# Kernel optimization log

Measured on AMD Instinct MI355X. Metric: run time of the kernel, lower is better.

## Reference

```python
import jax, jax.numpy as jnp
import numpy as np

B, LD, HD, CC, SC, PN, MAX_N = 256, 256, 512, 64, 256, 100000, 128


def setup_inputs() -> dict:
    key = jax.random.key(0)
    ks = jax.random.split(key, 24)
    def W(k, i, o):
        return jax.random.normal(k, (i, o), jnp.float32) * 0.02
    latent = jax.random.normal(ks[0], (B, LD), jnp.float32)
    n = jax.random.randint(ks[1], (B,), 0, MAX_N, jnp.int32)
    points = jax.random.normal(ks[2], (PN, SC), jnp.float32)
    a = jax.random.normal(ks[3], (PN, CC), jnp.float32)
    angles_params = a / (jnp.linalg.norm(a, axis=1, keepdims=True) + 1e-5)
    return {
        "latent": latent, "n": n, "points": points, "angles_params": angles_params,
        # angle_mlp: LD->HD->HD->HD->CC (4 linears, relu between)
        "aw1": W(ks[4], LD, HD), "ab1": jnp.zeros((HD,), jnp.float32),
        "aw2": W(ks[5], HD, HD), "ab2": jnp.zeros((HD,), jnp.float32),
        "aw3": W(ks[6], HD, HD), "ab3": jnp.zeros((HD,), jnp.float32),
        "aw4": W(ks[7], HD, CC), "ab4": jnp.zeros((CC,), jnp.float32),
        # lin1/lin2: 1 -> SC
        "l1w": W(ks[8], 1, SC), "l1b": jnp.zeros((SC,), jnp.float32),
        "l2w": W(ks[9], 1, SC), "l2b": jnp.zeros((SC,), jnp.float32),
        # out_lin: (SC+LD)->(SC+LD)->SC->SC
        "ow1": W(ks[10], SC + LD, SC + LD), "ob1": jnp.zeros((SC + LD,), jnp.float32),
        "ow2": W(ks[11], SC + LD, SC), "ob2": jnp.zeros((SC,), jnp.float32),
        "ow3": W(ks[12], SC, SC), "ob3": jnp.zeros((SC,), jnp.float32),
    }


def reference(latent, n, points, angles_params,
              aw1, ab1, aw2, ab2, aw3, ab3, aw4, ab4,
              l1w, l1b, l2w, l2b,
              ow1, ob1, ow2, ob2, ow3, ob3):
    n_r = jnp.clip(n, 1, MAX_N)  # round_n
    # angle_mlp
    h = jax.nn.relu(latent @ aw1 + ab1)
    h = jax.nn.relu(h @ aw2 + ab2)
    h = jax.nn.relu(h @ aw3 + ab3)
    ang = h @ aw4 + ab4                                   # [B, CC]
    ang = ang / (jnp.linalg.norm(ang, axis=1, keepdims=True) + 1e-5)
    cosine = jax.nn.softmax(ang @ angles_params.T, axis=1)  # [B, PN]
    srted, idx = jax.lax.top_k(cosine, MAX_N)             # sorted descending
    sel = points[idx]                                     # [B, MAX_N, SC] gather
    s = (MAX_N * srted)[..., None]                        # [B, MAX_N, 1]
    alpha = s @ l1w + l1b
    beta = s @ l2w + l2b
    mod = alpha * sel + beta                              # [B, MAX_N, SC]
    mask = (jnp.arange(MAX_N)[None, :] < n_r[:, None]).astype(jnp.float32)[..., None]
    cat = jnp.concatenate(
        [mod, jnp.broadcast_to(latent[:, None, :], (latent.shape[0], MAX_N, latent.shape[1]))],
        axis=-1)
    o = jax.nn.relu(cat @ ow1 + ob1)
    o = jax.nn.relu(o @ ow2 + ob2)
    out = o @ ow3 + ob3                                   # [B, MAX_N, SC]
    return out, mask, n_r
```

## Files before the change

kernel.cpp:

```cpp
#include <hip/hip_runtime.h>

#define PN 100000
#define NCB2 1563
#define NCBG 782
#define TSEL 0.33f
#define NSLOT 8
#define PREP_AP 3128
#define PREP_TOT 4408
#define PREP_CHUNK 1102

typedef _Float16 f16;
typedef _Float16 f16x8 __attribute__((ext_vector_type(8)));
typedef _Float16 f16x4 __attribute__((ext_vector_type(4)));
typedef float f32x4 __attribute__((ext_vector_type(4)));

__device__ __forceinline__ unsigned int sortkey(float f) {
    unsigned int u = __float_as_uint(f);
    return u ^ ((u & 0x80000000u) ? 0xFFFFFFFFu : 0x80000000u);
}

__device__ __forceinline__ void gload_lds16(const void* g, void* l) {
    __builtin_amdgcn_global_load_lds((const __attribute__((address_space(1))) void*)g,
                                     (__attribute__((address_space(3))) void*)l, 16, 0, 0);
}

__device__ __forceinline__ void prep_work(
    int pid, const float* __restrict__ ap, f16* __restrict__ apHpre, f16* __restrict__ apLpre,
    const float* __restrict__ ow1, const float* __restrict__ ow2, const float* __restrict__ ow3,
    f16* __restrict__ W1t, f16* __restrict__ W2t, f16* __restrict__ W3t)
{
    if (pid < PREP_AP) {
        int idx = pid * 256 + threadIdx.x;
        int gcol = idx >> 3, m = idx & 7;
        int bx = gcol >> 7, col = gcol & 127;
        size_t woff = (size_t)bx * 16384 + (size_t)col * 128 + (size_t)((m ^ (col & 7)) << 4);
        f16x8 h, l;
        if (gcol < PN) {
            const float* src = &ap[(size_t)gcol * 64 + m * 8];
            float4 a = *(const float4*)&src[0];
            float4 b = *(const float4*)&src[4];
            h[0] = (f16)a.x; l[0] = (f16)(a.x - (float)h[0]);
            h[1] = (f16)a.y; l[1] = (f16)(a.y - (float)h[1]);
            h[2] = (f16)a.z; l[2] = (f16)(a.z - (float)h[2]);
            h[3] = (f16)a.w; l[3] = (f16)(a.w - (float)h[3]);
            h[4] = (f16)b.x; l[4] = (f16)(b.x - (float)h[4]);
            h[5] = (f16)b.y; l[5] = (f16)(b.y - (float)h[5]);
            h[6] = (f16)b.z; l[6] = (f16)(b.z - (float)h[6]);
            h[7] = (f16)b.w; l[7] = (f16)(b.w - (float)h[7]);
        } else {
            h = (f16x8){}; l = (f16x8){};
        }
        *(f16x8*)((char*)apHpre + woff) = h;
        *(f16x8*)((char*)apLpre + woff) = l;
    } else {
        int idx = (pid - PREP_AP) * 256 + threadIdx.x;
        if (idx < 131072) {
            int n = idx >> 8, k = idx & 255;
            W1t[idx] = (f16)ow1[(size_t)k * 512 + n];
        } else if (idx < 262144) {
            int j = idx - 131072;
            int n = j >> 9, k = j & 511;
            W2t[j] = (f16)ow2[(size_t)k * 256 + n];
        } else {
            int j = idx - 262144;
            int n = j >> 8, k = j & 255;
            W3t[j] = (f16)ow3[(size_t)k * 256 + n];
        }
    }
}

template<int RELU>
__global__ __launch_bounds__(256) void k1_layer(
    const float* __restrict__ X, const float* __restrict__ W,
    const float* __restrict__ bias, float* __restrict__ Y,
    int N, int K, int prep_base,
    const float* __restrict__ ap, f16* __restrict__ apHpre, f16* __restrict__ apLpre,
    const float* __restrict__ ow1, const float* __restrict__ ow2, const float* __restrict__ ow3,
    f16* __restrict__ W1t, f16* __restrict__ W2t, f16* __restrict__ W3t)
{
    int bid = blockIdx.x;
    if (bid >= 128) {
        prep_work(prep_base + bid - 128, ap, apHpre, apLpre, ow1, ow2, ow3, W1t, W2t, W3t);
        return;
    }
    __shared__ __align__(16) float As[128][36];
    __shared__ __align__(16) float Bs[128][36];
    int t = threadIdx.x;
    int cbase = (bid & 15) * 32;
    int rbase = (bid >> 4) * 32;
    int tx = t & 7, ty = t >> 3;
    float acc[4] = {};

    for (int kt = 0; kt < K; kt += 128) {
        #pragma unroll
        for (int i = 0; i < 4; ++i) {
            int e = i * 256 + t;
            int r = e >> 5, k4 = e & 31;
            float4 v = *(const float4*)&X[(size_t)(rbase + r) * K + kt + k4 * 4];
            As[k4 * 4 + 0][r] = v.x; As[k4 * 4 + 1][r] = v.y;
            As[k4 * 4 + 2][r] = v.z; As[k4 * 4 + 3][r] = v.w;
        }
        #pragma unroll
        for (int i = 0; i < 4; ++i) {
            int e = i * 256 + t;
            int k = e >> 3, c4 = e & 7;
            *(float4*)&Bs[k][c4 * 4] = *(const float4*)&W[(size_t)(kt + k) * N + cbase + c4 * 4];
        }
        __syncthreads();
        #pragma unroll 8
        for (int k = 0; k < 128; ++k) {
            float av = As[k][ty];
            float4 bv = *(const float4*)&Bs[k][tx * 4];
            acc[0] = fmaf(av, bv.x, acc[0]);
            acc[1] = fmaf(av, bv.y, acc[1]);
            acc[2] = fmaf(av, bv.z, acc[2]);
            acc[3] = fmaf(av, bv.w, acc[3]);
        }
        __syncthreads();
    }
    int row = rbase + ty;
    #pragma unroll
    for (int j = 0; j < 4; ++j) {
        int col = cbase + tx * 4 + j;
        float v = acc[j] + bias[col];
        Y[(size_t)row * N + col] = RELU ? fmaxf(v, 0.f) : v;
    }
}

__global__ __launch_bounds__(256) void k1_tail(
    const float* __restrict__ X, const float* __restrict__ W4,
    const float* __restrict__ b4, f16* __restrict__ angH, f16* __restrict__ angL,
    const float* __restrict__ latent, const float* __restrict__ ow1lat,
    const float* __restrict__ ob1, float* __restrict__ Lc, int prep_base,
    const float* __restrict__ ap, f16* __restrict__ apHpre, f16* __restrict__ apLpre,
    const float* __restrict__ ow1, const float* __restrict__ ow2, const float* __restrict__ ow3,
    f16* __restrict__ W1t, f16* __restrict__ W2t, f16* __restrict__ W3t)
{
    if (blockIdx.x >= 72) {
        prep_work(prep_base + blockIdx.x - 72, ap, apHpre, apLpre, ow1, ow2, ow3, W1t, W2t, W3t);
        return;
    }
    __shared__ __align__(16) float As[128][36];
    __shared__ __align__(16) float Bs[128][68];
    int t = threadIdx.x;
    int tx = t & 15, ty = t >> 4;
    float acc[2][4] = {};

    if (blockIdx.x < 8) {
        int rbase = blockIdx.x * 32;
        for (int kt = 0; kt < 512; kt += 128) {
            #pragma unroll
            for (int i = 0; i < 4; ++i) {
                int e = i * 256 + t;
                int r = e >> 5, k4 = e & 31;
                float4 v = *(const float4*)&X[(size_t)(rbase + r) * 512 + kt + k4 * 4];
                As[k4 * 4 + 0][r] = v.x; As[k4 * 4 + 1][r] = v.y;
                As[k4 * 4 + 2][r] = v.z; As[k4 * 4 + 3][r] = v.w;
            }
            #pragma unroll
            for (int i = 0; i < 8; ++i) {
                int e = i * 256 + t;
                int k = e >> 4, c4 = e & 15;
                *(float4*)&Bs[k][c4 * 4] = *(const float4*)&W4[(size_t)(kt + k) * 64 + c4 * 4];
            }
            __syncthreads();
            #pragma unroll 8
            for (int k = 0; k < 128; ++k) {
                float2 av = *(const float2*)&As[k][ty * 2];
                float4 bv = *(const float4*)&Bs[k][tx * 4];
                acc[0][0] = fmaf(av.x, bv.x, acc[0][0]); acc[0][1] = fmaf(av.x, bv.y, acc[0][1]);
                acc[0][2] = fmaf(av.x, bv.z, acc[0][2]); acc[0][3] = fmaf(av.x, bv.w, acc[0][3]);
                acc[1][0] = fmaf(av.y, bv.x, acc[1][0]); acc[1][1] = fmaf(av.y, bv.y, acc[1][1]);
                acc[1][2] = fmaf(av.y, bv.z, acc[1][2]); acc[1][3] = fmaf(av.y, bv.w, acc[1][3]);
            }
            __syncthreads();
        }
        #pragma unroll
        for (int i = 0; i < 2; ++i) {
            float v[4];
            float ss = 0.f;
            #pragma unroll
            for (int j = 0; j < 4; ++j) {
                v[j] = acc[i][j] + b4[tx * 4 + j];
                ss = fmaf(v[j], v[j], ss);
            }
            ss += __shfl_xor(ss, 1); ss += __shfl_xor(ss, 2);
            ss += __shfl_xor(ss, 4); ss += __shfl_xor(ss, 8);
            float inv = 1.0f / (sqrtf(ss) + 1e-5f);
            int row = rbase + ty * 2 + i;
            f16x4 h, l;
            #pragma unroll
            for (int j = 0; j < 4; ++j) {
                float val = v[j] * inv;
                h[j] = (f16)val;
                l[j] = (f16)(val - (float)h[j]);
            }
            *(f16x4*)&angH[(size_t)row * 64 + tx * 4] = h;
            *(f16x4*)&angL[(size_t)row * 64 + tx * 4] = l;
        }
    } else {
        int bid = blockIdx.x - 8;
        int cbase = (bid & 7) * 64;
        int rbase = (bid >> 3) * 32;
        for (int kt = 0; kt < 256; kt += 128) {
            #pragma unroll
            for (int i = 0; i < 4; ++i) {
                int e = i * 256 + t;
                int r = e >> 5, k4 = e & 31;
                float4 v = *(const float4*)&latent[(size_t)(rbase + r) * 256 + kt + k4 * 4];
                As[k4 * 4 + 0][r] = v.x; As[k4 * 4 + 1][r] = v.y;
                As[k4 * 4 + 2][r] = v.z; As[k4 * 4 + 3][r] = v.w;
            }
            #pragma unroll
            for (int i = 0; i < 8; ++i) {
                int e = i * 256 + t;
                int k = e >> 4, c4 = e & 15;
                *(float4*)&Bs[k][c4 * 4] = *(const float4*)&ow1lat[(size_t)(kt + k) * 512 + cbase + c4 * 4];
            }
            __syncthreads();
            #pragma unroll 8
            for (int k = 0; k < 128; ++k) {
                float2 av = *(const float2*)&As[k][ty * 2];
                float4 bv = *(const float4*)&Bs[k][tx * 4];
                acc[0][0] = fmaf(av.x, bv.x, acc[0][0]); acc[0][1] = fmaf(av.x, bv.y, acc[0][1]);
                acc[0][2] = fmaf(av.x, bv.z, acc[0][2]); acc[0][3] = fmaf(av.x, bv.w, acc[0][3]);
                acc[1][0] = fmaf(av.y, bv.x, acc[1][0]); acc[1][1] = fmaf(av.y, bv.y, acc[1][1]);
                acc[1][2] = fmaf(av.y, bv.z, acc[1][2]); acc[1][3] = fmaf(av.y, bv.w, acc[1][3]);
            }
            __syncthreads();
        }
        #pragma unroll
        for (int i = 0; i < 2; ++i) {
            int row = rbase + ty * 2 + i;
            #pragma unroll
            for (int j = 0; j < 4; ++j) {
                int col = cbase + tx * 4 + j;
                Lc[(size_t)row * 512 + col] = acc[i][j] + ob1[col];
            }
        }
    }
}

__global__ __launch_bounds__(256) void k2v10(
    const f16* __restrict__ angH, const f16* __restrict__ angL,
    const f16* __restrict__ apHpre, const f16* __restrict__ apLpre,
    float* __restrict__ gsum, unsigned int* __restrict__ cnt_g,
    unsigned long long* __restrict__ slot_g)
{
    __shared__ __align__(16) f16 Bh[128 * 64], Bl[128 * 64];
    __shared__ float psum[64][2];
    int t = threadIdx.x;
    int lane = t & 63, wave = t >> 6;
    int bx = blockIdx.x;
    int cbase = bx * 128;
    int rbase = blockIdx.y * 64;
    int wr = wave >> 1, wc = wave & 1;

    {
        const char* srcH = (const char*)apHpre + (size_t)bx * 16384 + t * 16;
        const char* srcL = (const char*)apLpre + (size_t)bx * 16384 + t * 16;
        char* dstH = (char*)Bh + wave * 1024;
        char* dstL = (char*)Bl + wave * 1024;
        #pragma unroll
        for (int c = 0; c < 4; ++c) {
            gload_lds16(srcH + c * 4096, dstH + c * 4096);
            gload_lds16(srcL + c * 4096, dstL + c * 4096);
        }
    }
    __syncthreads();

    f32x4 acc[2][4] = {};
    #pragma unroll
    for (int ks = 0; ks < 2; ++ks) {
        int kk = ks * 32 + (lane >> 4) * 8;
        f16x8 ah[2], al[2], bh[4], bl[4];
        #pragma unroll
        for (int i = 0; i < 2; ++i) {
            int row = rbase + wr * 32 + i * 16 + (lane & 15);
            ah[i] = *(const f16x8*)&angH[(size_t)row * 64 + kk];
            al[i] = *(const f16x8*)&angL[(size_t)row * 64 + kk];
        }
        #pragma unroll
        for (int j = 0; j < 4; ++j) {
            int col = wc * 64 + j * 16 + (lane & 15);
            unsigned int offb = (unsigned int)(col * 128 + kk * 2) ^ (unsigned int)((col & 7) << 4);
            bh[j] = *(const f16x8*)((char*)Bh + offb);
            bl[j] = *(const f16x8*)((char*)Bl + offb);
        }
        #pragma unroll
        for (int i = 0; i < 2; ++i)
            #pragma unroll
            for (int j = 0; j < 4; ++j) {
                acc[i][j] = __builtin_amdgcn_mfma_f32_16x16x32_f16(ah[i], bh[j], acc[i][j], 0, 0, 0);
                acc[i][j] = __builtin_amdgcn_mfma_f32_16x16x32_f16(ah[i], bl[j], acc[i][j], 0, 0, 0);
                acc[i][j] = __builtin_amdgcn_mfma_f32_16x16x32_f16(al[i], bh[j], acc[i][j], 0, 0, 0);
            }
    }

    int tx = lane & 15;
    #pragma unroll
    for (int i = 0; i < 2; ++i) {
        #pragma unroll
        for (int r2 = 0; r2 < 4; ++r2) {
            int lrow = wr * 32 + i * 16 + ((lane >> 4) << 2) + r2;
            int grow = rbase + lrow;
            float s = 0.f;
            unsigned int lk[4], li[4];
            int c = 0;
            #pragma unroll
            for (int j = 0; j < 4; ++j) {
                int gc = cbase + wc * 64 + j * 16 + tx;
                if (gc < PN) {
                    float v = acc[i][j][r2];
                    s += __expf(v);
                    if (v >= TSEL) { lk[c] = sortkey(v); li[c] = (unsigned int)gc; ++c; }
                }
            }
            s += __shfl_xor(s, 1); s += __shfl_xor(s, 2);
            s += __shfl_xor(s, 4); s += __shfl_xor(s, 8);
            int incl = c;
            #pragma unroll
            for (int d = 1; d < 16; d <<= 1) {
                int up = __shfl_up(incl, (unsigned int)d, 16);
                if (tx >= d) incl += up;
            }
            int excl = incl - c;
            int unit = bx * 2 + wc;
            if (unit < NCB2) {
                size_t base = ((size_t)unit * 256 + grow) * NSLOT;
                for (int k = 0; k < c; ++k) {
                    int sp = excl + k;
                    if (sp < NSLOT)
                        slot_g[base + sp] = (((unsigned long long)lk[k]) << 32) | (unsigned int)(~li[k]);
                }
                if (tx == 15) cnt_g[(size_t)unit * 256 + grow] = (unsigned int)incl;
            }
            if (tx == 0) psum[lrow][wc] = s;
        }
    }
    __syncthreads();
    if (t < 64)
        gsum[(size_t)bx * 256 + rbase + t] = psum[t][0] + psum[t][1];
}

__global__ __launch_bounds__(1024) void k3v5(
    const unsigned int* __restrict__ cnt_g, const unsigned long long* __restrict__ slot_g,
    const float* __restrict__ gsum, const int* __restrict__ nin,
    const float* __restrict__ points,
    const float* __restrict__ l1w, const float* __restrict__ l1b,
    const float* __restrict__ l2w, const float* __restrict__ l2b,
    f16* __restrict__ Xmod, float* __restrict__ maskp, float* __restrict__ nrp)
{
    __shared__ float wsum[16];
    __shared__ float s_inv;
    __shared__ unsigned int ccnt;
    __shared__ unsigned long long arr[1024];
    __shared__ float sprob[128];
    __shared__ int spi[128];
    __shared__ float sw1[256], sb1[256], sw2[256], sb2[256];

    int r = blockIdx.x;
    int t = threadIdx.x;
    if (t == 0) ccnt = 0u;
    if (t < 256) { sw1[t] = l1w[t]; sb1[t] = l1b[t]; sw2[t] = l2w[t]; sb2[t] = l2b[t]; }
    float es = 0.f;
    for (int i = t; i < NCBG; i += 1024) es += gsum[(size_t)i * 256 + r];
    #pragma unroll
    for (int off = 32; off > 0; off >>= 1) es += __shfl_xor(es, off);
    if ((t & 63) == 0) wsum[t >> 6] = es;
    __syncthreads();
    if (t == 0) {
        float s = 0.f;
        for (int i = 0; i < 16; ++i) s += wsum[i];
        s_inv = 1.0f / s;
    }
    for (int i = t; i < NCB2; i += 1024) {
        unsigned int c = cnt_g[(size_t)i * 256 + r];
        if (c) {
            c = min(c, (unsigned int)NSLOT);
            unsigned int p = atomicAdd(&ccnt, c);
            size_t base = ((size_t)i * 256 + r) * NSLOT;
            for (unsigned int k = 0; k < c; ++k)
                if (p + k < 1024u) arr[p + k] = slot_g[base + k];
        }
    }
    __syncthreads();
    int nc = (int)min(ccnt, 1024u);
    int P = 128;
    while (P < nc) P <<= 1;
    for (int i = t; i < P; i += 1024)
        if (i >= nc) arr[i] = 0ull;
    __syncthreads();
    for (int kk = 2; kk <= P; kk <<= 1) {
        for (int j = kk >> 1; j > 0; j >>= 1) {
            if (t < P) {
                int l = t ^ j;
                if (l > t) {
                    unsigned long long a = arr[t], b = arr[l];
                    bool up = ((t & kk) == 0);
                    if (up ? (a < b) : (a > b)) { arr[t] = b; arr[l] = a; }
                }
            }
            __syncthreads();
        }
    }
    int nr = nin[r]; nr = nr < 1 ? 1 : (nr > 128 ? 128 : nr);
    if (t < 128) {
        unsigned long long c = arr[t];
        unsigned int key = (unsigned int)(c >> 32);
        unsigned int idx = ~((unsigned int)c);
        if (idx >= PN) idx = 0;
        unsigned int u = (key & 0x80000000u) ? (key ^ 0x80000000u) : ~key;
        float v = __uint_as_float(u);
        sprob[t] = expf(v) * s_inv;
        spi[t] = (int)idx;
        maskp[r * 128 + t] = (t < nr) ? 1.0f : 0.0f;
    }
    if (t == 0) nrp[r] = (float)nr;
    __syncthreads();
    {
        int tok = t >> 3;
        int d0 = (t & 7) * 32;
        float s = 128.0f * sprob[tok];
        const float* prow = points + (size_t)spi[tok] * 256;
        f16* xrow = Xmod + ((size_t)(r * 128 + tok)) * 256;
        #pragma unroll
        for (int j = 0; j < 32; j += 4) {
            int d = d0 + j;
            float4 p = *(const float4*)&prow[d];
            f16x4 h;
            h[0] = (f16)fmaf(fmaf(s, sw1[d + 0], sb1[d + 0]), p.x, fmaf(s, sw2[d + 0], sb2[d + 0]));
            h[1] = (f16)fmaf(fmaf(s, sw1[d + 1], sb1[d + 1]), p.y, fmaf(s, sw2[d + 1], sb2[d + 1]));
            h[2] = (f16)fmaf(fmaf(s, sw1[d + 2], sb1[d + 2]), p.z, fmaf(s, sw2[d + 2], sb2[d + 2]));
            h[3] = (f16)fmaf(fmaf(s, sw1[d + 3], sb1[d + 3]), p.w, fmaf(s, sw2[d + 3], sb2[d + 3]));
            *(f16x4*)&xrow[d] = h;
        }
    }
}

template<int RELU, int OUT_F16, int LCBIAS>
__global__ __launch_bounds__(256) void gemm_tn3(
    const f16* __restrict__ A, const f16* __restrict__ Bt,
    const float* __restrict__ bias,
    f16* __restrict__ Cf16, float* __restrict__ Cf32,
    int N, int K)
{
    __shared__ __align__(16) f16 As[64 * 64];
    __shared__ __align__(16) f16 Bs[128 * 64];
    int tid = threadIdx.x;
    int lane = tid & 63, wave = tid >> 6;
    int brow = blockIdx.y * 64;
    int bcol = blockIdx.x * 128;
    int wr = wave >> 1, wc = wave & 1;

    f32x4 acc[2][4] = {};

    int sr = tid >> 3;
    int soff = (tid & 7) * 16;
    char* ldsA = (char*)As + wave * 1024;
    char* ldsB = (char*)Bs + wave * 1024;

    for (int kt = 0; kt < K; kt += 64) {
        #pragma unroll
        for (int c = 0; c < 2; ++c) {
            int r = sr + c * 32;
            const char* ga = (const char*)A + ((size_t)(brow + r) * K + kt) * 2 + soff;
            gload_lds16(ga, ldsA + c * 4096);
        }
        #pragma unroll
        for (int c = 0; c < 4; ++c) {
            int r = sr + c * 32;
            const char* gb = (const char*)Bt + ((size_t)(bcol + r) * K + kt) * 2 + soff;
            gload_lds16(gb, ldsB + c * 4096);
        }
        __syncthreads();
        #pragma unroll
        for (int ks = 0; ks < 2; ++ks) {
            f16x8 af[2], bf[4];
            int kk = ks * 32 + (lane >> 4) * 8;
            #pragma unroll
            for (int i = 0; i < 2; ++i) {
                int row = wr * 32 + i * 16 + (lane & 15);
                af[i] = *(const f16x8*)&As[row * 64 + kk];
            }
            #pragma unroll
            for (int j = 0; j < 4; ++j) {
                int col = wc * 64 + j * 16 + (lane & 15);
                bf[j] = *(const f16x8*)&Bs[col * 64 + kk];
            }
            #pragma unroll
            for (int i = 0; i < 2; ++i)
                #pragma unroll
                for (int j = 0; j < 4; ++j)
                    acc[i][j] = __builtin_amdgcn_mfma_f32_16x16x32_f16(af[i], bf[j], acc[i][j], 0, 0, 0);
        }
        __syncthreads();
    }

    #pragma unroll
    for (int i = 0; i < 2; ++i) {
        int row0 = brow + wr * 32 + i * 16 + (lane >> 4) * 4;
        #pragma unroll
        for (int j = 0; j < 4; ++j) {
            int col = bcol + wc * 64 + j * 16 + (lane & 15);
            float bz = LCBIAS ? bias[(size_t)(row0 >> 7) * N + col] : bias[col];
            #pragma unroll
            for (int r2 = 0; r2 < 4; ++r2) {
                float v = acc[i][j][r2] + bz;
                if (RELU) v = fmaxf(v, 0.f);
                if (OUT_F16) Cf16[(size_t)(row0 + r2) * N + col] = (f16)v;
                else         Cf32[(size_t)(row0 + r2) * N + col] = v;
            }
        }
    }
}

extern "C" void kernel_launch(void* const* d_in, const int* in_sizes, int n_in,
                              void* d_out, int out_size, void* d_ws, size_t ws_size,
                              hipStream_t stream) {
    (void)in_sizes; (void)n_in; (void)out_size; (void)ws_size;
    const float* latent = (const float*)d_in[0];
    const int*   nin    = (const int*)d_in[1];
    const float* points = (const float*)d_in[2];
    const float* ap     = (const float*)d_in[3];
    const float* aw1 = (const float*)d_in[4];  const float* ab1 = (const float*)d_in[5];
    const float* aw2 = (const float*)d_in[6];  const float* ab2 = (const float*)d_in[7];
    const float* aw3 = (const float*)d_in[8];  const float* ab3 = (const float*)d_in[9];
    const float* aw4 = (const float*)d_in[10]; const float* ab4 = (const float*)d_in[11];
    const float* l1w = (const float*)d_in[12]; const float* l1b = (const float*)d_in[13];
    const float* l2w = (const float*)d_in[14]; const float* l2b = (const float*)d_in[15];
    const float* ow1 = (const float*)d_in[16]; const float* ob1 = (const float*)d_in[17];
    const float* ow2 = (const float*)d_in[18]; const float* ob2 = (const float*)d_in[19];
    const float* ow3 = (const float*)d_in[20]; const float* ob3 = (const float*)d_in[21];

    char* wsb = (char*)d_ws;
    f16* angH  = (f16*)wsb;
    f16* angL  = (f16*)(wsb + 65536);
    unsigned int* cnt_g = (unsigned int*)(wsb + 1048576);
    float* gsum   = (float*)(wsb + 3145728);
    float* h1 = (float*)(wsb + 5242880);
    float* h2 = (float*)(wsb + 5767168);
    float* h3 = (float*)(wsb + 6291456);
    float* Lc = (float*)(wsb + 6815744);
    f16* apHpre = (f16*)(wsb + 8388608);
    f16* Xmod = (f16*)(wsb + 8388608);
    unsigned long long* slot_g = (unsigned long long*)(wsb + 25165824);
    f16* H1  = (f16*)(wsb + 25165824);
    f16* apLpre = (f16*)(wsb + 58720256);
    f16* H2  = (f16*)(wsb + 58720256);
    f16* W1t = (f16*)(wsb + 75497472);
    f16* W2t = (f16*)(wsb + 75759616);
    f16* W3t = (f16*)(wsb + 76021760);

    float* outp  = (float*)d_out;
    float* maskp = outp + 8388608;
    float* nrp   = outp + 8421376;

    hipLaunchKernelGGL((k1_layer<1>), dim3(128 + PREP_CHUNK), dim3(256), 0, stream,
                       latent, aw1, ab1, h1, 512, 256, 0,
                       ap, apHpre, apLpre, ow1, ow2, ow3, W1t, W2t, W3t);
    hipLaunchKernelGGL((k1_layer<1>), dim3(128 + PREP_CHUNK), dim3(256), 0, stream,
                       h1, aw2, ab2, h2, 512, 512, PREP_CHUNK,
                       ap, apHpre, apLpre, ow1, ow2, ow3, W1t, W2t, W3t);
    hipLaunchKernelGGL((k1_layer<1>), dim3(128 + PREP_CHUNK), dim3(256), 0, stream,
                       h2, aw3, ab3, h3, 512, 512, 2 * PREP_CHUNK,
                       ap, apHpre, apLpre, ow1, ow2, ow3, W1t, W2t, W3t);
    hipLaunchKernelGGL(k1_tail, dim3(72 + PREP_CHUNK), dim3(256), 0, stream,
                       h3, aw4, ab4, angH, angL,
                       latent, ow1 + (size_t)256 * 512, ob1, Lc, 3 * PREP_CHUNK,
                       ap, apHpre, apLpre, ow1, ow2, ow3, W1t, W2t, W3t);
    hipLaunchKernelGGL(k2v10, dim3(NCBG, 4), dim3(256), 0, stream,
                       angH, angL, apHpre, apLpre, gsum, cnt_g, slot_g);
    hipLaunchKernelGGL(k3v5, dim3(256), dim3(1024), 0, stream,
                       cnt_g, slot_g, gsum, nin, points, l1w, l1b, l2w, l2b,
                       Xmod, maskp, nrp);
    hipLaunchKernelGGL((gemm_tn3<1, 1, 1>), dim3(4, 512), dim3(256), 0, stream,
                       Xmod, W1t, Lc, H1, (float*)nullptr, 512, 256);
    hipLaunchKernelGGL((gemm_tn3<1, 1, 0>), dim3(2, 512), dim3(256), 0, stream,
                       H1, W2t, ob2, H2, (float*)nullptr, 256, 512);
    hipLaunchKernelGGL((gemm_tn3<0, 0, 0>), dim3(2, 512), dim3(256), 0, stream,
                       H2, W3t, ob3, (f16*)nullptr, outp, 256, 256);
}
```

Baseline: 177.4 us.

## Fuse three output MLP GEMMs into one kernel keeping activations in LDS

Replaces the three separate gemm_tn3 launches with a single gemm_fused kernel in which each 512-thread block owns 64 rows and keeps its layer-1 and layer-2 activations in shared memory. This removes the global round trips for H1 and H2 and two kernel launches. Weights and the Xmod input are pre-packed into swizzled 64x64 tiles, so loads go straight to LDS without bank conflicts, and the weight prep is vectorised to f16x8 stores. In exchange the grid has only 512 blocks, each using about 96KB of LDS, which limits occupancy, and the weight tile loads are single-buffered with two barriers per step.

```diff
diff --git a/kernel.cpp b/kernel.cpp
--- a/kernel.cpp
+++ b/kernel.cpp
@@ -6,8 +6,9 @@
 #define TSEL 0.33f
 #define NSLOT 8
 #define PREP_AP 3128
-#define PREP_TOT 4408
-#define PREP_CHUNK 1102
+#define PREP_W 160
+#define PREP_TOT 3288
+#define PREP_CHUNK 822
 
 typedef _Float16 f16;
 typedef _Float16 f16x8 __attribute__((ext_vector_type(8)));
@@ -27,7 +28,7 @@
 __device__ __forceinline__ void prep_work(
     int pid, const float* __restrict__ ap, f16* __restrict__ apHpre, f16* __restrict__ apLpre,
     const float* __restrict__ ow1, const float* __restrict__ ow2, const float* __restrict__ ow3,
-    f16* __restrict__ W1t, f16* __restrict__ W2t, f16* __restrict__ W3t)
+    f16* __restrict__ W1p, f16* __restrict__ W2p, f16* __restrict__ W3p)
 {
     if (pid < PREP_AP) {
         int idx = pid * 256 + threadIdx.x;
@@ -53,19 +54,37 @@
         *(f16x8*)((char*)apHpre + woff) = h;
         *(f16x8*)((char*)apLpre + woff) = l;
     } else {
-        int idx = (pid - PREP_AP) * 256 + threadIdx.x;
-        if (idx < 131072) {
-            int n = idx >> 8, k = idx & 255;
-            W1t[idx] = (f16)ow1[(size_t)k * 512 + n];
-        } else if (idx < 262144) {
-            int j = idx - 131072;
-            int n = j >> 9, k = j & 511;
-            W2t[j] = (f16)ow2[(size_t)k * 256 + n];
+        int gid = (pid - PREP_AP) * 256 + threadIdx.x;
+        f16x8 h;
+        char* dst;
+        if (gid < 16384) {
+            int n = gid >> 5, k0 = (gid & 31) * 8;
+            const float* src = ow1 + (size_t)k0 * 512 + n;
+            #pragma unroll
+            for (int m = 0; m < 8; ++m) h[m] = (f16)src[(size_t)m * 512];
+            int nin = n & 127;
+            unsigned int off = ((unsigned int)(nin * 128 + (k0 & 63) * 2)) ^ ((unsigned int)((nin & 7) << 4));
+            dst = (char*)W1p + (size_t)((n >> 7) * 4 + (k0 >> 6)) * 16384 + off;
+        } else if (gid < 32768) {
+            int g = gid - 16384;
+            int n = g >> 6, k0 = (g & 63) * 8;
+            const float* src = ow2 + (size_t)k0 * 256 + n;
+            #pragma unroll
+            for (int m = 0; m < 8; ++m) h[m] = (f16)src[(size_t)m * 256];
+            int nin = n & 127;
+            unsigned int off = ((unsigned int)(nin * 128 + (k0 & 63) * 2)) ^ ((unsigned int)((nin & 7) << 4));
+            dst = (char*)W2p + (size_t)((n >> 7) * 8 + (k0 >> 6)) * 16384 + off;
         } else {
-            int j = idx - 262144;
-            int n = j >> 8, k = j & 255;
-            W3t[j] = (f16)ow3[(size_t)k * 256 + n];
-        }
+            int g = gid - 32768;
+            int n = g >> 5, k0 = (g & 31) * 8;
+            const float* src = ow3 + (size_t)k0 * 256 + n;
+            #pragma unroll
+            for (int m = 0; m < 8; ++m) h[m] = (f16)src[(size_t)m * 256];
+            int nin = n & 127;
+            unsigned int off = ((unsigned int)(nin * 128 + (k0 & 63) * 2)) ^ ((unsigned int)((nin & 7) << 4));
+            dst = (char*)W3p + (size_t)((n >> 7) * 4 + (k0 >> 6)) * 16384 + off;
+        }
+        *(f16x8*)dst = h;
     }
 }
 
@@ -76,11 +95,11 @@
     int N, int K, int prep_base,
     const float* __restrict__ ap, f16* __restrict__ apHpre, f16* __restrict__ apLpre,
     const float* __restrict__ ow1, const float* __restrict__ ow2, const float* __restrict__ ow3,
-    f16* __restrict__ W1t, f16* __restrict__ W2t, f16* __restrict__ W3t)
+    f16* __restrict__ W1p, f16* __restrict__ W2p, f16* __restrict__ W3p)
 {
     int bid = blockIdx.x;
     if (bid >= 128) {
-        prep_work(prep_base + bid - 128, ap, apHpre, apLpre, ow1, ow2, ow3, W1t, W2t, W3t);
+        prep_work(prep_base + bid - 128, ap, apHpre, apLpre, ow1, ow2, ow3, W1p, W2p, W3p);
         return;
     }
     __shared__ __align__(16) float As[128][36];
@@ -134,10 +153,10 @@
     const float* __restrict__ ob1, float* __restrict__ Lc, int prep_base,
     const float* __restrict__ ap, f16* __restrict__ apHpre, f16* __restrict__ apLpre,
     const float* __restrict__ ow1, const float* __restrict__ ow2, const float* __restrict__ ow3,
-    f16* __restrict__ W1t, f16* __restrict__ W2t, f16* __restrict__ W3t)
+    f16* __restrict__ W1p, f16* __restrict__ W2p, f16* __restrict__ W3p)
 {
     if (blockIdx.x >= 72) {
-        prep_work(prep_base + blockIdx.x - 72, ap, apHpre, apLpre, ow1, ow2, ow3, W1t, W2t, W3t);
+        prep_work(prep_base + blockIdx.x - 72, ap, apHpre, apLpre, ow1, ow2, ow3, W1p, W2p, W3p);
         return;
     }
     __shared__ __align__(16) float As[128][36];
@@ -349,7 +368,7 @@
     const float* __restrict__ points,
     const float* __restrict__ l1w, const float* __restrict__ l1b,
     const float* __restrict__ l2w, const float* __restrict__ l2b,
-    f16* __restrict__ Xmod, float* __restrict__ maskp, float* __restrict__ nrp)
+    f16* __restrict__ Xmp, float* __restrict__ maskp, float* __restrict__ nrp)
 {
     __shared__ float wsum[16];
     __shared__ float s_inv;
@@ -423,7 +442,10 @@
         int d0 = (t & 7) * 32;
         float s = 128.0f * sprob[tok];
         const float* prow = points + (size_t)spi[tok] * 256;
-        f16* xrow = Xmod + ((size_t)(r * 128 + tok)) * 256;
+        int tile = r * 2 + (tok >> 6);
+        int rowin = tok & 63;
+        char* xbase = (char*)Xmp + (size_t)tile * 32768;
+        unsigned int sw = (unsigned int)((rowin & 7) << 4);
         #pragma unroll
         for (int j = 0; j < 32; j += 4) {
             int d = d0 + j;
@@ -433,85 +455,183 @@
             h[1] = (f16)fmaf(fmaf(s, sw1[d + 1], sb1[d + 1]), p.y, fmaf(s, sw2[d + 1], sb2[d + 1]));
             h[2] = (f16)fmaf(fmaf(s, sw1[d + 2], sb1[d + 2]), p.z, fmaf(s, sw2[d + 2], sb2[d + 2]));
             h[3] = (f16)fmaf(fmaf(s, sw1[d + 3], sb1[d + 3]), p.w, fmaf(s, sw2[d + 3], sb2[d + 3]));
-            *(f16x4*)&xrow[d] = h;
-        }
-    }
-}
-
-template<int RELU, int OUT_F16, int LCBIAS>
-__global__ __launch_bounds__(256) void gemm_tn3(
-    const f16* __restrict__ A, const f16* __restrict__ Bt,
-    const float* __restrict__ bias,
-    f16* __restrict__ Cf16, float* __restrict__ Cf32,
-    int N, int K)
+            unsigned int off = ((unsigned int)((d >> 6) * 8192)) +
+                               (((unsigned int)(rowin * 128 + (d & 63) * 2)) ^ sw);
+            *(f16x4*)(xbase + off) = h;
+        }
+    }
+}
+
+__global__ __launch_bounds__(512) void gemm_fused(
+    const f16* __restrict__ Xmp, const f16* __restrict__ W1p,
+    const f16* __restrict__ W2p, const f16* __restrict__ W3p,
+    const float* __restrict__ Lc, const float* __restrict__ ob2,
+    const float* __restrict__ ob3, float* __restrict__ outp)
 {
-    __shared__ __align__(16) f16 As[64 * 64];
-    __shared__ __align__(16) f16 Bs[128 * 64];
-    int tid = threadIdx.x;
-    int lane = tid & 63, wave = tid >> 6;
-    int brow = blockIdx.y * 64;
-    int bcol = blockIdx.x * 128;
-    int wr = wave >> 1, wc = wave & 1;
-
-    f32x4 acc[2][4] = {};
-
-    int sr = tid >> 3;
-    int soff = (tid & 7) * 16;
-    char* ldsA = (char*)As + wave * 1024;
-    char* ldsB = (char*)Bs + wave * 1024;
-
-    for (int kt = 0; kt < K; kt += 64) {
-        #pragma unroll
-        for (int c = 0; c < 2; ++c) {
-            int r = sr + c * 32;
-            const char* ga = (const char*)A + ((size_t)(brow + r) * K + kt) * 2 + soff;
-            gload_lds16(ga, ldsA + c * 4096);
-        }
-        #pragma unroll
-        for (int c = 0; c < 4; ++c) {
-            int r = sr + c * 32;
-            const char* gb = (const char*)Bt + ((size_t)(bcol + r) * K + kt) * 2 + soff;
-            gload_lds16(gb, ldsB + c * 4096);
-        }
-        __syncthreads();
-        #pragma unroll
-        for (int ks = 0; ks < 2; ++ks) {
-            f16x8 af[2], bf[4];
-            int kk = ks * 32 + (lane >> 4) * 8;
-            #pragma unroll
-            for (int i = 0; i < 2; ++i) {
-                int row = wr * 32 + i * 16 + (lane & 15);
-                af[i] = *(const f16x8*)&As[row * 64 + kk];
-            }
-            #pragma unroll
-            for (int j = 0; j < 4; ++j) {
-                int col = wc * 64 + j * 16 + (lane & 15);
-                bf[j] = *(const f16x8*)&Bs[col * 64 + kk];
-            }
-            #pragma unroll
-            for (int i = 0; i < 2; ++i)
-                #pragma unroll
-                for (int j = 0; j < 4; ++j)
-                    acc[i][j] = __builtin_amdgcn_mfma_f32_16x16x32_f16(af[i], bf[j], acc[i][j], 0, 0, 0);
-        }
-        __syncthreads();
-    }
-
-    #pragma unroll
-    for (int i = 0; i < 2; ++i) {
-        int row0 = brow + wr * 32 + i * 16 + (lane >> 4) * 4;
-        #pragma unroll
-        for (int j = 0; j < 4; ++j) {
-            int col = bcol + wc * 64 + j * 16 + (lane & 15);
-            float bz = LCBIAS ? bias[(size_t)(row0 >> 7) * N + col] : bias[col];
-            #pragma unroll
-            for (int r2 = 0; r2 < 4; ++r2) {
-                float v = acc[i][j][r2] + bz;
-                if (RELU) v = fmaxf(v, 0.f);
-                if (OUT_F16) Cf16[(size_t)(row0 + r2) * N + col] = (f16)v;
-                else         Cf32[(size_t)(row0 + r2) * N + col] = v;
-            }
-        }
+    __shared__ __align__(16) f16 Xs[4 * 64 * 64];
+    __shared__ __align__(16) f16 Hs[8 * 64 * 64];
+    __shared__ __align__(16) f16 Wb[128 * 64];
+    int t = threadIdx.x;
+    int lane = t & 63, wave = t >> 6;
+    int wr = wave >> 2, wc = wave & 3;
+    int bid = blockIdx.x;
+    int r0 = bid * 64;
+    int lcr = bid >> 1;
+
+    {
+        const char* src = (const char*)Xmp + (size_t)bid * 32768 + t * 16;
+        char* dst = (char*)Xs + wave * 1024;
+        #pragma unroll
+        for (int c = 0; c < 4; ++c)
+            gload_lds16(src + c * 8192, dst + c * 8192);
+    }
+
+    for (int cc = 0; cc < 4; ++cc) {
+        f32x4 acc[2][2] = {};
+        for (int kt = 0; kt < 4; ++kt) {
+            __syncthreads();
+            {
+                const char* src = (const char*)W1p + (size_t)(cc * 4 + kt) * 16384 + t * 16;
+                char* dst = (char*)Wb + wave * 1024;
+                gload_lds16(src, dst);
+                gload_lds16(src + 8192, dst + 8192);
+            }
+            __syncthreads();
+            #pragma unroll
+            for (int ks = 0; ks < 2; ++ks) {
+                int kk = ks * 32 + (lane >> 4) * 8;
+                f16x8 af[2], bf[2];
+                #pragma unroll
+                for (int i = 0; i < 2; ++i) {
+                    int row = wr * 32 + i * 16 + (lane & 15);
+                    unsigned int off = ((unsigned int)(row * 128 + kk * 2)) ^ ((unsigned int)((row & 7) << 4));
+                    af[i] = *(const f16x8*)((const char*)Xs + kt * 8192 + off);
+                }
+                #pragma unroll
+                for (int j = 0; j < 2; ++j) {
+                    int nr2 = wc * 32 + j * 16 + (lane & 15);
+                    unsigned int off = ((unsigned int)(nr2 * 128 + kk * 2)) ^ ((unsigned int)((nr2 & 7) << 4));
+                    bf[j] = *(const f16x8*)((const char*)Wb + off);
+                }
+                #pragma unroll
+                for (int i = 0; i < 2; ++i)
+                    #pragma unroll
+                    for (int j = 0; j < 2; ++j)
+                        acc[i][j] = __builtin_amdgcn_mfma_f32_16x16x32_f16(af[i], bf[j], acc[i][j], 0, 0, 0);
+            }
+        }
+        #pragma unroll
+        for (int i = 0; i < 2; ++i)
+            #pragma unroll
+            for (int j = 0; j < 2; ++j) {
+                int col = cc * 128 + wc * 32 + j * 16 + (lane & 15);
+                float bz = Lc[(size_t)lcr * 512 + col];
+                #pragma unroll
+                for (int r2 = 0; r2 < 4; ++r2) {
+                    int row = wr * 32 + i * 16 + ((lane >> 4) << 2) + r2;
+                    float v = fmaxf(acc[i][j][r2] + bz, 0.f);
+                    unsigned int off = ((unsigned int)(row * 128 + (col & 63) * 2)) ^ ((unsigned int)((row & 7) << 4));
+                    *(f16*)((char*)Hs + (col >> 6) * 8192 + off) = (f16)v;
+                }
+            }
+    }
+
+    for (int cc = 0; cc < 2; ++cc) {
+        f32x4 acc[2][2] = {};
+        for (int kt = 0; kt < 8; ++kt) {
+            __syncthreads();
+            {
+                const char* src = (const char*)W2p + (size_t)(cc * 8 + kt) * 16384 + t * 16;
+                char* dst = (char*)Wb + wave * 1024;
+                gload_lds16(src, dst);
+                gload_lds16(src + 8192, dst + 8192);
+            }
+            __syncthreads();
+            #pragma unroll
+            for (int ks = 0; ks < 2; ++ks) {
+                int kk = ks * 32 + (lane >> 4) * 8;
+                f16x8 af[2], bf[2];
+                #pragma unroll
+                for (int i = 0; i < 2; ++i) {
+                    int row = wr * 32 + i * 16 + (lane & 15);
+                    unsigned int off = ((unsigned int)(row * 128 + kk * 2)) ^ ((unsigned int)((row & 7) << 4));
+                    af[i] = *(const f16x8*)((const char*)Hs + kt * 8192 + off);
+                }
+                #pragma unroll
+                for (int j = 0; j < 2; ++j) {
+                    int nr2 = wc * 32 + j * 16 + (lane & 15);
+                    unsigned int off = ((unsigned int)(nr2 * 128 + kk * 2)) ^ ((unsigned int)((nr2 & 7) << 4));
+                    bf[j] = *(const f16x8*)((const char*)Wb + off);
+                }
+                #pragma unroll
+                for (int i = 0; i < 2; ++i)
+                    #pragma unroll
+                    for (int j = 0; j < 2; ++j)
+                        acc[i][j] = __builtin_amdgcn_mfma_f32_16x16x32_f16(af[i], bf[j], acc[i][j], 0, 0, 0);
+            }
+        }
+        #pragma unroll
+        for (int i = 0; i < 2; ++i)
+            #pragma unroll
+            for (int j = 0; j < 2; ++j) {
+                int col = cc * 128 + wc * 32 + j * 16 + (lane & 15);
+                float bz = ob2[col];
+                #pragma unroll
+                for (int r2 = 0; r2 < 4; ++r2) {
+                    int row = wr * 32 + i * 16 + ((lane >> 4) << 2) + r2;
+                    float v = fmaxf(acc[i][j][r2] + bz, 0.f);
+                    unsigned int off = ((unsigned int)(row * 128 + (col & 63) * 2)) ^ ((unsigned int)((row & 7) << 4));
+                    *(f16*)((char*)Xs + (col >> 6) * 8192 + off) = (f16)v;
+                }
+            }
+    }
+
+    for (int cc = 0; cc < 2; ++cc) {
+        f32x4 acc[2][2] = {};
+        for (int kt = 0; kt < 4; ++kt) {
+            __syncthreads();
+            {
+                const char* src = (const char*)W3p + (size_t)(cc * 4 + kt) * 16384 + t * 16;
+                char* dst = (char*)Wb + wave * 1024;
+                gload_lds16(src, dst);
+                gload_lds16(src + 8192, dst + 8192);
+            }
+            __syncthreads();
+            #pragma unroll
+            for (int ks = 0; ks < 2; ++ks) {
+                int kk = ks * 32 + (lane >> 4) * 8;
+                f16x8 af[2], bf[2];
+                #pragma unroll
+                for (int i = 0; i < 2; ++i) {
+                    int row = wr * 32 + i * 16 + (lane & 15);
+                    unsigned int off = ((unsigned int)(row * 128 + kk * 2)) ^ ((unsigned int)((row & 7) << 4));
+                    af[i] = *(const f16x8*)((const char*)Xs + kt * 8192 + off);
+                }
+                #pragma unroll
+                for (int j = 0; j < 2; ++j) {
+                    int nr2 = wc * 32 + j * 16 + (lane & 15);
+                    unsigned int off = ((unsigned int)(nr2 * 128 + kk * 2)) ^ ((unsigned int)((nr2 & 7) << 4));
+                    bf[j] = *(const f16x8*)((const char*)Wb + off);
+                }
+                #pragma unroll
+                for (int i = 0; i < 2; ++i)
+                    #pragma unroll
+                    for (int j = 0; j < 2; ++j)
+                        acc[i][j] = __builtin_amdgcn_mfma_f32_16x16x32_f16(af[i], bf[j], acc[i][j], 0, 0, 0);
+            }
+        }
+        #pragma unroll
+        for (int i = 0; i < 2; ++i)
+            #pragma unroll
+            for (int j = 0; j < 2; ++j) {
+                int col = cc * 128 + wc * 32 + j * 16 + (lane & 15);
+                float bz = ob3[col];
+                #pragma unroll
+                for (int r2 = 0; r2 < 4; ++r2) {
+                    int row = wr * 32 + i * 16 + ((lane >> 4) << 2) + r2;
+                    outp[(size_t)(r0 + row) * 256 + col] = acc[i][j][r2] + bz;
+                }
+            }
     }
 }
 
@@ -543,14 +663,12 @@
     float* h3 = (float*)(wsb + 6291456);
     float* Lc = (float*)(wsb + 6815744);
     f16* apHpre = (f16*)(wsb + 8388608);
-    f16* Xmod = (f16*)(wsb + 8388608);
+    f16* Xmp = (f16*)(wsb + 8388608);
     unsigned long long* slot_g = (unsigned long long*)(wsb + 25165824);
-    f16* H1  = (f16*)(wsb + 25165824);
     f16* apLpre = (f16*)(wsb + 58720256);
-    f16* H2  = (f16*)(wsb + 58720256);
-    f16* W1t = (f16*)(wsb + 75497472);
-    f16* W2t = (f16*)(wsb + 75759616);
-    f16* W3t = (f16*)(wsb + 76021760);
+    f16* W1p = (f16*)(wsb + 75497472);
+    f16* W2p = (f16*)(wsb + 75759616);
+    f16* W3p = (f16*)(wsb + 76021760);
 
     float* outp  = (float*)d_out;
     float* maskp = outp + 8388608;
@@ -558,26 +676,22 @@
 
     hipLaunchKernelGGL((k1_layer<1>), dim3(128 + PREP_CHUNK), dim3(256), 0, stream,
                        latent, aw1, ab1, h1, 512, 256, 0,
-                       ap, apHpre, apLpre, ow1, ow2, ow3, W1t, W2t, W3t);
+                       ap, apHpre, apLpre, ow1, ow2, ow3, W1p, W2p, W3p);
     hipLaunchKernelGGL((k1_layer<1>), dim3(128 + PREP_CHUNK), dim3(256), 0, stream,
                        h1, aw2, ab2, h2, 512, 512, PREP_CHUNK,
-                       ap, apHpre, apLpre, ow1, ow2, ow3, W1t, W2t, W3t);
+                       ap, apHpre, apLpre, ow1, ow2, ow3, W1p, W2p, W3p);
     hipLaunchKernelGGL((k1_layer<1>), dim3(128 + PREP_CHUNK), dim3(256), 0, stream,
                        h2, aw3, ab3, h3, 512, 512, 2 * PREP_CHUNK,
-                       ap, apHpre, apLpre, ow1, ow2, ow3, W1t, W2t, W3t);
+                       ap, apHpre, apLpre, ow1, ow2, ow3, W1p, W2p, W3p);
     hipLaunchKernelGGL(k1_tail, dim3(72 + PREP_CHUNK), dim3(256), 0, stream,
                        h3, aw4, ab4, angH, angL,
                        latent, ow1 + (size_t)256 * 512, ob1, Lc, 3 * PREP_CHUNK,
-                       ap, apHpre, apLpre, ow1, ow2, ow3, W1t, W2t, W3t);
+                       ap, apHpre, apLpre, ow1, ow2, ow3, W1p, W2p, W3p);
     hipLaunchKernelGGL(k2v10, dim3(NCBG, 4), dim3(256), 0, stream,
                        angH, angL, apHpre, apLpre, gsum, cnt_g, slot_g);
     hipLaunchKernelGGL(k3v5, dim3(256), dim3(1024), 0, stream,
                        cnt_g, slot_g, gsum, nin, points, l1w, l1b, l2w, l2b,
-                       Xmod, maskp, nrp);
-    hipLaunchKernelGGL((gemm_tn3<1, 1, 1>), dim3(4, 512), dim3(256), 0, stream,
-                       Xmod, W1t, Lc, H1, (float*)nullptr, 512, 256);
-    hipLaunchKernelGGL((gemm_tn3<1, 1, 0>), dim3(2, 512), dim3(256), 0, stream,
-                       H1, W2t, ob2, H2, (float*)nullptr, 256, 512);
-    hipLaunchKernelGGL((gemm_tn3<0, 0, 0>), dim3(2, 512), dim3(256), 0, stream,
-                       H2, W3t, ob3, (f16*)nullptr, outp, 256, 256);
-}
+                       Xmp, maskp, nrp);
+    hipLaunchKernelGGL(gemm_fused, dim3(512), dim3(512), 0, stream,
+                       Xmp, W1p, W2p, W3p, Lc, ob2, ob3, outp);
+}
```

New measurement: 184.4 us. 4.0% more time.
